# Performance work log

Measured on AMD Instinct MI355X. Metric: run time of the kernel, lower is better.

Reference implementation:

```python
import jax, jax.numpy as jnp
import numpy as np

B, T, D, H, L = 512, 1024, 2, 32, 16  # batch, seq_len, input_dim, hidden_dim, latent_dim


def lstm_layer(x, W_ih, W_hh, b_ih, b_hh):
    """Single torch-semantics LSTM layer. x: [B, T, D_in] -> (h_seq [B,T,H], c_final [B,H]).
    Gate order matches torch: i, f, g, o."""
    Bb = x.shape[0]
    Hh = W_hh.shape[1]
    # Precompute input projection for all timesteps (one big GEMM).
    xW = jnp.einsum('btd,gd->btg', x, W_ih) + (b_ih + b_hh)  # [B, T, 4H]

    def step(carry, xw_t):
        h, c = carry
        gates = xw_t + h @ W_hh.T  # [B, 4H]
        i, f, g, o = jnp.split(gates, 4, axis=-1)
        i = jax.nn.sigmoid(i)
        f = jax.nn.sigmoid(f)
        g = jnp.tanh(g)
        o = jax.nn.sigmoid(o)
        c = f * c + i * g
        h = o * jnp.tanh(c)
        return (h, c), h

    h0 = jnp.zeros((Bb, Hh), x.dtype)
    c0 = jnp.zeros((Bb, Hh), x.dtype)
    (_, cT), h_seq = jax.lax.scan(step, (h0, c0), jnp.swapaxes(xW, 0, 1))
    return jnp.swapaxes(h_seq, 0, 1), cT


def setup_inputs() -> dict:
    key = jax.random.key(0)
    ks = jax.random.split(key, 20)
    s = 1.0 / np.sqrt(H)  # torch LSTM/Linear init scale
    u = lambda k, shape: jax.random.uniform(k, shape, jnp.float32, -s, s)
    inp = {"x": jax.random.normal(ks[0], (B, T, D), jnp.float32)}
    dims_in = [D, H, H]
    for l in range(3):
        inp[f"W_ih{l}"] = u(ks[1 + 4 * l], (4 * H, dims_in[l]))
        inp[f"W_hh{l}"] = u(ks[2 + 4 * l], (4 * H, H))
        inp[f"b_ih{l}"] = u(ks[3 + 4 * l], (4 * H,))
        inp[f"b_hh{l}"] = u(ks[4 + 4 * l], (4 * H,))
    inp["W_mean"] = u(ks[13], (L, H))
    inp["b_mean"] = u(ks[14], (L,))
    inp["W_logvar"] = u(ks[15], (L, H))
    inp["b_logvar"] = u(ks[16], (L,))
    return inp


def reference(x, W_ih0, W_hh0, b_ih0, b_hh0, W_ih1, W_hh1, b_ih1, b_hh1,
              W_ih2, W_hh2, b_ih2, b_hh2, W_mean, b_mean, W_logvar, b_logvar):
    # 3-layer LSTM (dropout inactive at inference); only top-layer final cell is used.
    h, _ = lstm_layer(x, W_ih0, W_hh0, b_ih0, b_hh0)
    h, _ = lstm_layer(h, W_ih1, W_hh1, b_ih1, b_hh1)
    _, c3 = lstm_layer(h, W_ih2, W_hh2, b_ih2, b_hh2)  # c3: [B, H]
    mean = c3 @ W_mean.T + b_mean        # [B, L]
    log_var = c3 @ W_logvar.T + b_logvar  # [B, L]
    return (mean, log_var)
```

## Files before the change

kernel.cpp:

```cpp
#include <hip/hip_runtime.h>

#define T_LEN 1024
#define HID   32
#define LDIM  16
#define BATCH 512
#define NB    16
#define NT    768
#define ROWB  80
#define SLOTB (16 * ROWB)
#define PARB  (4 * SLOTB)
#define LOG2E 1.44269504f

typedef _Float16 half8  __attribute__((ext_vector_type(8)));
typedef _Float16 half2v __attribute__((ext_vector_type(2)));
typedef float    f32x4  __attribute__((ext_vector_type(4)));
typedef unsigned u32;
typedef unsigned u32x4  __attribute__((ext_vector_type(4)));

#if defined(__has_builtin)
#if __has_builtin(__builtin_amdgcn_rcpf)
#define FAST_RCP(x) __builtin_amdgcn_rcpf(x)
#endif
#if __has_builtin(__builtin_amdgcn_exp2f)
#define FAST_EXP2(x) __builtin_amdgcn_exp2f(x)
#endif
#if __has_builtin(__builtin_amdgcn_cvt_pkrtz)
#define PKRTZ(a, b) __builtin_bit_cast(u32, __builtin_amdgcn_cvt_pkrtz((a), (b)))
#endif
#endif
#ifndef FAST_RCP
#define FAST_RCP(x) (1.0f / (x))
#endif
#ifndef FAST_EXP2
#define FAST_EXP2(x) __expf(0.69314718f * (x))
#endif
#ifndef PKRTZ
static __device__ __forceinline__ u32 pkrtz_fallback(float a, float b) {
    half2v v; v[0] = (_Float16)a; v[1] = (_Float16)b;
    return __builtin_bit_cast(u32, v);
}
#define PKRTZ(a, b) pkrtz_fallback((a), (b))
#endif

#define MFMA(a, b, c) __builtin_amdgcn_mfma_f32_16x16x32_f16((a), (b), (c), 0, 0, 0)

__global__ __launch_bounds__(NT, 1)
void lstm_encoder_kernel(const float* __restrict__ x,
                         const float* __restrict__ Wih0, const float* __restrict__ Whh0,
                         const float* __restrict__ bih0, const float* __restrict__ bhh0,
                         const float* __restrict__ Wih1, const float* __restrict__ Whh1,
                         const float* __restrict__ bih1, const float* __restrict__ bhh1,
                         const float* __restrict__ Wih2, const float* __restrict__ Whh2,
                         const float* __restrict__ bih2, const float* __restrict__ bhh2,
                         const float* __restrict__ Wm,  const float* __restrict__ bm,
                         const float* __restrict__ Wlv, const float* __restrict__ blv,
                         float* __restrict__ out)
{
    const int b0   = blockIdx.x * NB;
    const int tid  = threadIdx.x;
    const int lane = tid & 63;
    const int wave = tid >> 6;
    const int l    = wave >> 2;
    const int w    = wave & 3;
    const int n    = lane & 15;
    const int kc   = lane >> 4;

    __shared__ u32 xs[T_LEN * NB];
    __shared__ __align__(16) unsigned char hb[2 * PARB];
    __shared__ float cbuf[NB * HID];

    for (int i = tid; i < NB * T_LEN; i += NT) {
        const int nn = i >> 10, t = i & (T_LEN - 1);
        const float2 v = *(const float2*)(x + ((size_t)(b0 + nn) * T_LEN + t) * 2);
        half2v p; p[0] = (_Float16)v.x; p[1] = (_Float16)v.y;
        xs[t * NB + nn] = __builtin_bit_cast(u32, p);
    }
    for (int i = tid; i < (int)(2 * PARB / 4); i += NT) ((u32*)hb)[i] = 0u;

    const float* Wih = (l == 0) ? Wih0 : (l == 1) ? Wih1 : Wih2;
    const float* Whh = (l == 0) ? Whh0 : (l == 1) ? Whh1 : Whh2;
    const float* bih = (l == 0) ? bih0 : (l == 1) ? bih1 : bih2;
    const float* bhh = (l == 0) ? bhh0 : (l == 1) ? bhh1 : bhh2;

    half8 aprev[2], aself[2];
    f32x4 biasC[2];
#pragma unroll
    for (int tau = 0; tau < 2; ++tau) {
        const int   rho  = n & 1, uloc = n >> 1;
        const int   base = (tau == 0) ? (rho ? 32 : 0) : (rho ? 96 : 64);
        const int   R    = base + 8 * w + uloc;
        const float sc   = (tau == 1 && rho == 0) ? (2.0f * LOG2E) : LOG2E;
#pragma unroll
        for (int i2 = 0; i2 < 8; ++i2) {
            const int kk = kc * 8 + i2;
            aself[tau][i2] = (_Float16)(Whh[R * HID + kk] * sc);
            aprev[tau][i2] = (_Float16)(((l == 0) ? ((kk < 2) ? Wih[R * 2 + kk] : 0.0f)
                                                  : Wih[R * HID + kk]) * sc);
        }
#pragma unroll
        for (int r = 0; r < 4; ++r) {
            const int   rr    = r & 1, uD = 2 * kc + (r >> 1);
            const int   baseD = (tau == 0) ? (rr ? 32 : 0) : (rr ? 96 : 64);
            const int   RD    = baseD + 8 * w + uD;
            const float scD   = (tau == 1 && rr == 0) ? (2.0f * LOG2E) : LOG2E;
            biasC[tau][r] = (bih[RD] + bhh[RD]) * scD;
        }
    }

    const int slotA  = (l == 0) ? 3 : (l - 1);
    const int off_r0 = slotA * SLOTB + n * ROWB + kc * 16;
    const int off_r1 = l * SLOTB + n * ROWB + kc * 16;
    const int off_w  = l * SLOTB + n * ROWB + (8 * w + 2 * kc) * 2;
    const int off_x  = 3 * SLOTB + lane * ROWB;
    const bool xf    = (wave == 0) && (lane < 16);

    float cc0 = 0.0f, cc1 = 0.0f;

    __syncthreads();
    if (xf) *(u32*)(hb + off_x) = xs[lane];
    __syncthreads();

#define CELL(ai, af_, ag, ao, CC, HOUT)                                          \
    do {                                                                         \
        const float ei = FAST_EXP2(-(ai));                                       \
        const float ef = FAST_EXP2(-(af_));                                      \
        const float eg = FAST_EXP2(-(ag));                                       \
        const float eo = FAST_EXP2(-(ao));                                       \
        const float p1  = (1.0f + ei) * (1.0f + eg);                             \
        const float den = p1 * (1.0f + ef);                                      \
        const float tmn = (1.0f - eg) * (1.0f + ef);                             \
        float c_ = fmaf(CC, p1, tmn) * FAST_RCP(den);                            \
        c_ = fminf(fmaxf(c_, -20.0f), 20.0f);                                    \
        CC = c_;                                                                 \
        const float ec = FAST_EXP2(-2.0f * LOG2E * c_);                          \
        HOUT = (1.0f - ec) * FAST_RCP((1.0f + eo) * (1.0f + ec));                \
    } while (0)

#define STEP(P, S)                                                               \
    do {                                                                         \
        if ((unsigned)((S) - l) < (unsigned)T_LEN) {                             \
            u32 xw = 0;                                                          \
            if (xf) {                                                            \
                const int tn = ((S) + 1 < T_LEN) ? (S) + 1 : T_LEN - 1;          \
                xw = xs[tn * NB + lane];                                         \
            }                                                                    \
            const half8 bf0 = __builtin_bit_cast(half8,                          \
                *(const u32x4*)(hb + (P) * PARB + off_r0));                      \
            const half8 bf1 = __builtin_bit_cast(half8,                          \
                *(const u32x4*)(hb + (P) * PARB + off_r1));                      \
            f32x4 ac0 = MFMA(aprev[0], bf0, biasC[0]);                           \
            f32x4 ac1 = MFMA(aprev[1], bf0, biasC[1]);                           \
            ac0 = MFMA(aself[0], bf1, ac0);                                      \
            ac1 = MFMA(aself[1], bf1, ac1);                                      \
            float h0, h1;                                                        \
            CELL(ac0[0], ac0[1], ac1[0], ac1[1], cc0, h0);                       \
            CELL(ac0[2], ac0[3], ac1[2], ac1[3], cc1, h1);                       \
            *(u32*)(hb + ((P) ^ 1) * PARB + off_w) = PKRTZ(h0, h1);              \
            if (xf) *(u32*)(hb + ((P) ^ 1) * PARB + off_x) = xw;                 \
        }                                                                        \
        __syncthreads();                                                         \
    } while (0)

    for (int s = 0; s < T_LEN + 2; s += 2) {
        STEP(0, s);
        STEP(1, s + 1);
    }
#undef STEP
#undef CELL

    if (l == 2) {
        cbuf[n * HID + 8 * w + 2 * kc + 0] = cc0;
        cbuf[n * HID + 8 * w + 2 * kc + 1] = cc1;
    }
    __syncthreads();

    if (tid < NB * 2 * LDIM) {
        const int  nn = tid >> 5;
        const int  o  = tid & 31;
        const bool is_mean = (o < LDIM);
        const int  jo = o & (LDIM - 1);
        const float* W  = is_mean ? Wm : Wlv;
        float acc = is_mean ? bm[jo] : blv[jo];
#pragma unroll
        for (int k = 0; k < HID; ++k) acc = fmaf(W[jo * HID + k], cbuf[nn * HID + k], acc);
        out[(is_mean ? 0 : (size_t)BATCH * LDIM) + (size_t)(b0 + nn) * LDIM + jo] = acc;
    }
}

extern "C" void kernel_launch(void* const* d_in, const int* in_sizes, int n_in,
                              void* d_out, int out_size, void* d_ws, size_t ws_size,
                              hipStream_t stream) {
    const float* x    = (const float*)d_in[0];
    const float* Wih0 = (const float*)d_in[1];
    const float* Whh0 = (const float*)d_in[2];
    const float* bih0 = (const float*)d_in[3];
    const float* bhh0 = (const float*)d_in[4];
    const float* Wih1 = (const float*)d_in[5];
    const float* Whh1 = (const float*)d_in[6];
    const float* bih1 = (const float*)d_in[7];
    const float* bhh1 = (const float*)d_in[8];
    const float* Wih2 = (const float*)d_in[9];
    const float* Whh2 = (const float*)d_in[10];
    const float* bih2 = (const float*)d_in[11];
    const float* bhh2 = (const float*)d_in[12];
    const float* Wm   = (const float*)d_in[13];
    const float* bm   = (const float*)d_in[14];
    const float* Wlv  = (const float*)d_in[15];
    const float* blv  = (const float*)d_in[16];
    float* out = (float*)d_out;

    lstm_encoder_kernel<<<dim3(BATCH / NB), dim3(NT), 0, stream>>>(
        x, Wih0, Whh0, bih0, bhh0, Wih1, Whh1, bih1, bhh1,
        Wih2, Whh2, bih2, bhh2, Wm, bm, Wlv, blv, out);
}
```

Measured before the change: 519.6 us.

## Replace per-step block barriers with LDS ring buffer and per-layer atomic counters

The lockstep double-buffered schedule, which ran one __syncthreads per timestep across all 12 waves, becomes an 8-slot LDS ring buffer. Point-to-point waits use workgroup-scope atomic counters per layer. Each layer's waves now wait only on their own layer's previous step, the lower layer's current output, and ring-slot reuse by the upper layer. The aim is to let layers drift apart and drop the cost of full-workgroup barriers. The trade-off is spin-polling with s_sleep and atomic traffic on the critical recurrence path.

After: 490.3 us. 5.6% less time.

```diff
diff --git a/kernel.cpp b/kernel.cpp
--- a/kernel.cpp
+++ b/kernel.cpp
@@ -8,7 +8,8 @@
 #define NT    768
 #define ROWB  80
 #define SLOTB (16 * ROWB)
-#define PARB  (4 * SLOTB)
+#define SLOT_ALL (4 * SLOTB)
+#define NSLOT 8
 #define LOG2E 1.44269504f
 
 typedef _Float16 half8  __attribute__((ext_vector_type(8)));
@@ -43,6 +44,11 @@
 #endif
 
 #define MFMA(a, b, c) __builtin_amdgcn_mfma_f32_16x16x32_f16((a), (b), (c), 0, 0, 0)
+
+__device__ __forceinline__ void waitc(const u32* p, u32 need) {
+    while (__hip_atomic_load(p, __ATOMIC_ACQUIRE, __HIP_MEMORY_SCOPE_WORKGROUP) < need)
+        __builtin_amdgcn_s_sleep(1);
+}
 
 __global__ __launch_bounds__(NT, 1)
 void lstm_encoder_kernel(const float* __restrict__ x,
@@ -66,7 +72,8 @@
     const int kc   = lane >> 4;
 
     __shared__ u32 xs[T_LEN * NB];
-    __shared__ __align__(16) unsigned char hb[2 * PARB];
+    __shared__ __align__(16) unsigned char ring[NSLOT * SLOT_ALL];
+    __shared__ u32 cnt[48];
     __shared__ float cbuf[NB * HID];
 
     for (int i = tid; i < NB * T_LEN; i += NT) {
@@ -75,7 +82,8 @@
         half2v p; p[0] = (_Float16)v.x; p[1] = (_Float16)v.y;
         xs[t * NB + nn] = __builtin_bit_cast(u32, p);
     }
-    for (int i = tid; i < (int)(2 * PARB / 4); i += NT) ((u32*)hb)[i] = 0u;
+    for (int i = tid; i < (int)(sizeof(ring) / 4); i += NT) ((u32*)ring)[i] = 0u;
+    if (tid < 48) cnt[tid] = 0u;
 
     const float* Wih = (l == 0) ? Wih0 : (l == 1) ? Wih1 : Wih2;
     const float* Whh = (l == 0) ? Whh0 : (l == 1) ? Whh1 : Whh2;
@@ -107,17 +115,20 @@
         }
     }
 
-    const int slotA  = (l == 0) ? 3 : (l - 1);
-    const int off_r0 = slotA * SLOTB + n * ROWB + kc * 16;
+    const int off_r0 = ((l == 0) ? 3 : (l - 1)) * SLOTB + n * ROWB + kc * 16;
     const int off_r1 = l * SLOTB + n * ROWB + kc * 16;
     const int off_w  = l * SLOTB + n * ROWB + (8 * w + 2 * kc) * 2;
     const int off_x  = 3 * SLOTB + lane * ROWB;
     const bool xf    = (wave == 0) && (lane < 16);
 
+    u32* cs = &cnt[l * 16];
+    u32* cp = &cnt[((l > 0) ? (l - 1) : 0) * 16];
+    u32* cn = &cnt[((l < 2) ? (l + 1) : 0) * 16];
+
     float cc0 = 0.0f, cc1 = 0.0f;
 
     __syncthreads();
-    if (xf) *(u32*)(hb + off_x) = xs[lane];
+    if (xf) *(u32*)(ring + off_x) = xs[lane];
     __syncthreads();
 
 #define CELL(ai, af_, ag, ao, CC, HOUT)                                          \
@@ -136,36 +147,41 @@
         HOUT = (1.0f - ec) * FAST_RCP((1.0f + eo) * (1.0f + ec));                \
     } while (0)
 
-#define STEP(P, S)                                                               \
-    do {                                                                         \
-        if ((unsigned)((S) - l) < (unsigned)T_LEN) {                             \
-            u32 xw = 0;                                                          \
-            if (xf) {                                                            \
-                const int tn = ((S) + 1 < T_LEN) ? (S) + 1 : T_LEN - 1;          \
-                xw = xs[tn * NB + lane];                                         \
-            }                                                                    \
-            const half8 bf0 = __builtin_bit_cast(half8,                          \
-                *(const u32x4*)(hb + (P) * PARB + off_r0));                      \
-            const half8 bf1 = __builtin_bit_cast(half8,                          \
-                *(const u32x4*)(hb + (P) * PARB + off_r1));                      \
-            f32x4 ac0 = MFMA(aprev[0], bf0, biasC[0]);                           \
-            f32x4 ac1 = MFMA(aprev[1], bf0, biasC[1]);                           \
-            ac0 = MFMA(aself[0], bf1, ac0);                                      \
-            ac1 = MFMA(aself[1], bf1, ac1);                                      \
-            float h0, h1;                                                        \
-            CELL(ac0[0], ac0[1], ac1[0], ac1[1], cc0, h0);                       \
-            CELL(ac0[2], ac0[3], ac1[2], ac1[3], cc1, h1);                       \
-            *(u32*)(hb + ((P) ^ 1) * PARB + off_w) = PKRTZ(h0, h1);              \
-            if (xf) *(u32*)(hb + ((P) ^ 1) * PARB + off_x) = xw;                 \
-        }                                                                        \
-        __syncthreads();                                                         \
-    } while (0)
-
-    for (int s = 0; s < T_LEN + 2; s += 2) {
-        STEP(0, s);
-        STEP(1, s + 1);
-    }
-#undef STEP
+    for (int tb = 0; tb < T_LEN; tb += NSLOT) {
+#pragma unroll
+        for (int s = 0; s < NSLOT; ++s) {
+            const int t = tb + s;
+            if (t > 0)                 waitc(cs, 4u * (u32)t);
+            if (l > 0)                 waitc(cp, 4u * (u32)(t + 1));
+            if (l < 2 && t >= NSLOT)   waitc(cn, 4u * (u32)(t - 7));
+
+            u32 xw = 0;
+            if (xf) {
+                const int tn = (t + 1 < T_LEN) ? (t + 1) : (T_LEN - 1);
+                xw = xs[tn * NB + lane];
+            }
+            const half8 bf0 = __builtin_bit_cast(half8,
+                *(const u32x4*)(ring + s * SLOT_ALL + off_r0));
+            const half8 bf1 = __builtin_bit_cast(half8,
+                *(const u32x4*)(ring + ((s + 7) & 7) * SLOT_ALL + off_r1));
+
+            f32x4 ac0 = MFMA(aprev[0], bf0, biasC[0]);
+            f32x4 ac1 = MFMA(aprev[1], bf0, biasC[1]);
+            ac0 = MFMA(aself[0], bf1, ac0);
+            ac1 = MFMA(aself[1], bf1, ac1);
+
+            float h0, h1;
+            CELL(ac0[0], ac0[1], ac1[0], ac1[1], cc0, h0);
+            CELL(ac0[2], ac0[3], ac1[2], ac1[3], cc1, h1);
+
+            *(u32*)(ring + s * SLOT_ALL + off_w) = PKRTZ(h0, h1);
+            if (xf) *(u32*)(ring + ((s + 1) & 7) * SLOT_ALL + off_x) = xw;
+
+            if (lane == 0)
+                __hip_atomic_fetch_add(cs, 1u, __ATOMIC_RELEASE,
+                                       __HIP_MEMORY_SCOPE_WORKGROUP);
+        }
+    }
 #undef CELL
 
     if (l == 2) {
```
